# Kernel tuning notes

Measured on AMD Instinct MI355X. Metric: run time of the kernel, lower is better.

## Reference

```python
import jax, jax.numpy as jnp
import numpy as np

B, S, D, H = 4, 2048, 512, 8
DK = D // H


def setup_inputs() -> dict:
    key = jax.random.key(0)
    k1, k2, k3, k4 = jax.random.split(key, 4)
    return {
        "Zq": jax.random.normal(k1, (B, S, D), dtype=jnp.float32),
        "Zkv": jax.random.normal(k2, (B, S, D), dtype=jnp.float32),
        "mask": jnp.zeros((1, 1, S, S), dtype=jnp.float32),
        "Wqkv": jax.random.normal(k3, (D, 3 * D), dtype=jnp.float32),
        "Wout": jax.random.normal(k4, (D, D), dtype=jnp.float32),
    }


def reference(Zq, Zkv, mask, Wqkv, Wout):
    d_k = Wqkv.shape[0] // H
    Wq, Wk, Wv = jnp.split(Wqkv, 3, axis=-1)
    b, s, d = Zq.shape
    # project and split heads: [B,S,D] -> [B,H,S,dk]
    Q = (Zq @ Wq).reshape(b, s, H, d_k).transpose(0, 2, 1, 3)
    K = (Zkv @ Wk).reshape(b, s, H, d_k).transpose(0, 2, 1, 3)
    V = (Zkv @ Wv).reshape(b, s, H, d_k).transpose(0, 2, 1, 3)
    scale = d_k ** -0.5
    scores = jnp.einsum("bhqd,bhkd->bhqk", Q, K) * scale + mask
    attn = jax.nn.softmax(scores, axis=-1)  # [B,H,Sq,Skv]
    ctx = jnp.einsum("bhqk,bhkd->bhqd", attn, V)
    out = ctx.transpose(0, 2, 1, 3).reshape(b, s, d) @ Wout
    return out, attn.mean(axis=1)
```

## Files before the change

### kernel.cpp

```cpp
#include <hip/hip_runtime.h>
#include <cstdint>
#include <math.h>

#define B_ 4
#define S_ 2048
#define D_ 512
#define H_ 8
#define DK_ 64
#define SCALE 0.125f
#define INVLN2 1.4426950408889634f
#define QSCALE (SCALE * INVLN2)
#define KSTR 84
#define PSTR 68

using bfrag = __attribute__((ext_vector_type(8))) __bf16;
using b4    = __attribute__((ext_vector_type(4))) __bf16;
using f4    = __attribute__((ext_vector_type(4))) float;
using f2    = __attribute__((ext_vector_type(2))) float;
using f16v  = __attribute__((ext_vector_type(16))) float;
using u2    = __attribute__((ext_vector_type(2))) unsigned int;

#define MFMA16(a, b, c) __builtin_amdgcn_mfma_f32_16x16x32_bf16(a, b, c, 0, 0, 0)
#define MFMA32(a, b, c) __builtin_amdgcn_mfma_f32_32x32x16_bf16(a, b, c, 0, 0, 0)

__global__ __launch_bounds__(256) void wtr_all(
    const float* __restrict__ Wqkv, const float* __restrict__ Wout,
    __bf16* __restrict__ WqTh, __bf16* __restrict__ WqTl,
    __bf16* __restrict__ WkTh, __bf16* __restrict__ WkTl,
    __bf16* __restrict__ WvTh, __bf16* __restrict__ WoTh) {
  const int by = blockIdx.y;
  const int idx = blockIdx.x * 256 + threadIdx.x;
  const int k = idx & 511, n = idx >> 9;
  const float* W = (by == 3) ? Wout : Wqkv;
  const int ldw = (by == 3) ? 512 : 1536;
  const int c0 = (by == 3) ? 0 : by * 512;
  const float x = W[(size_t)k * ldw + c0 + n];
  const __bf16 h = (__bf16)x;
  __bf16* th = (by == 0) ? WqTh : (by == 1) ? WkTh : (by == 2) ? WvTh : WoTh;
  th[(size_t)n * 512 + k] = h;
  if (by < 2) {
    __bf16* tl = (by == 0) ? WqTl : WkTl;
    tl[(size_t)n * 512 + k] = (__bf16)(x - (float)h);
  }
}

__global__ __launch_bounds__(256) void qk_proj(
    const float* __restrict__ Zq, const float* __restrict__ Zkv,
    const __bf16* __restrict__ WqTh, const __bf16* __restrict__ WqTl,
    const __bf16* __restrict__ WkTh, const __bf16* __restrict__ WkTl,
    __bf16* __restrict__ Qh, __bf16* __restrict__ Ql,
    __bf16* __restrict__ Kh, __bf16* __restrict__ Kl) {
  __shared__ __bf16 Ash[64 * 40];
  __shared__ __bf16 Asl[64 * 40];
  __shared__ __bf16 Bsh[64 * 40];
  __shared__ __bf16 Bsl[64 * 40];

  const int zz = blockIdx.z;
  const float* A = zz ? Zkv : Zq;
  const __bf16* Bhp = zz ? WkTh : WqTh;
  const __bf16* Blp = zz ? WkTl : WqTl;
  __bf16* Oh = zz ? Kh : Qh;
  __bf16* Ol = zz ? Kl : Ql;
  const float cs = zz ? 1.0f : QSCALE;

  const int tid = threadIdx.x;
  const int m0 = blockIdx.y * 64, n0 = blockIdx.x * 64;
  const int row = tid >> 2, seg = tid & 3;
  const int lane = tid & 63, wv = tid >> 6;
  const int wm = (wv & 1) * 32, wn = (wv >> 1) * 32;
  const int qd = lane >> 4, ln = lane & 15;

  f4 acc[2][2];
#pragma unroll
  for (int i = 0; i < 2; i++)
#pragma unroll
    for (int j = 0; j < 2; j++)
#pragma unroll
      for (int r = 0; r < 4; r++) acc[i][j][r] = 0.f;

  for (int kt = 0; kt < 512; kt += 32) {
    const size_t abase = (size_t)(m0 + row) * 512 + kt + seg * 8;
    const size_t bbase = (size_t)(n0 + row) * 512 + kt + seg * 8;
    float4 a0 = *(const float4*)&A[abase];
    float4 a1 = *(const float4*)&A[abase + 4];
    float4 b0 = *(const float4*)&Bhp[bbase];
    float4 bl0 = *(const float4*)&Blp[bbase];
    __syncthreads();
    {
      float x[8] = {a0.x, a0.y, a0.z, a0.w, a1.x, a1.y, a1.z, a1.w};
      bfrag h, l;
#pragma unroll
      for (int j = 0; j < 8; j++) {
        h[j] = (__bf16)x[j];
        l[j] = (__bf16)(x[j] - (float)h[j]);
      }
      *(bfrag*)&Ash[row * 40 + seg * 8] = h;
      *(bfrag*)&Asl[row * 40 + seg * 8] = l;
    }
    *(float4*)&Bsh[row * 40 + seg * 8] = b0;
    *(float4*)&Bsl[row * 40 + seg * 8] = bl0;
    __syncthreads();

    bfrag ah[2], al[2], bh[2], bl[2];
#pragma unroll
    for (int mi = 0; mi < 2; mi++) {
      ah[mi] = *(bfrag*)&Ash[(wm + mi * 16 + ln) * 40 + qd * 8];
      al[mi] = *(bfrag*)&Asl[(wm + mi * 16 + ln) * 40 + qd * 8];
    }
#pragma unroll
    for (int ni = 0; ni < 2; ni++) {
      bh[ni] = *(bfrag*)&Bsh[(wn + ni * 16 + ln) * 40 + qd * 8];
      bl[ni] = *(bfrag*)&Bsl[(wn + ni * 16 + ln) * 40 + qd * 8];
    }
#pragma unroll
    for (int mi = 0; mi < 2; mi++)
#pragma unroll
      for (int ni = 0; ni < 2; ni++) {
        acc[mi][ni] = MFMA16(ah[mi], bh[ni], acc[mi][ni]);
        acc[mi][ni] = MFMA16(ah[mi], bl[ni], acc[mi][ni]);
        acc[mi][ni] = MFMA16(al[mi], bh[ni], acc[mi][ni]);
      }
  }

#pragma unroll
  for (int mi = 0; mi < 2; mi++)
#pragma unroll
    for (int ni = 0; ni < 2; ni++)
#pragma unroll
      for (int r = 0; r < 4; r++) {
        const int mrow = m0 + wm + mi * 16 + qd * 4 + r;
        const int ncol = n0 + wn + ni * 16 + ln;
        const float c = acc[mi][ni][r] * cs;
        const int b = mrow >> 11, s = mrow & (S_ - 1);
        const int h = ncol >> 6, dk = ncol & 63;
        const size_t o = (((size_t)b * H_ + h) * S_ + s) * DK_ + dk;
        __bf16 hh = (__bf16)c;
        Oh[o] = hh;
        Ol[o] = (__bf16)(c - (float)hh);
      }
}

template <bool AF32, bool BF32, bool LO, int MODE>
__global__ __launch_bounds__(256) void gemm_mfma(
    const void* __restrict__ Ap, const void* __restrict__ Bp, const void* __restrict__ Blop,
    float* __restrict__ Cf, __bf16* __restrict__ Oh, __bf16* __restrict__ Ol) {
  __shared__ __bf16 Ash[64 * 40];
  __shared__ __bf16 Asl[64 * 40];
  __shared__ __bf16 Bsh[64 * 40];
  __shared__ __bf16 Bsl[64 * 40];

  const int tid = threadIdx.x;
  const int m0 = blockIdx.y * 64, n0 = blockIdx.x * 64;
  const int row = tid >> 2, seg = tid & 3;
  const int lane = tid & 63, wv = tid >> 6;
  const int wm = (wv & 1) * 32, wn = (wv >> 1) * 32;
  const int qd = lane >> 4, ln = lane & 15;

  f4 acc[2][2];
#pragma unroll
  for (int i = 0; i < 2; i++)
#pragma unroll
    for (int j = 0; j < 2; j++)
#pragma unroll
      for (int r = 0; r < 4; r++) acc[i][j][r] = 0.f;

  for (int kt = 0; kt < 512; kt += 32) {
    const size_t abase = (size_t)(m0 + row) * 512 + kt + seg * 8;
    const size_t bbase = (size_t)(n0 + row) * 512 + kt + seg * 8;
    float4 a0, a1, b0, b1, bl0;
    if constexpr (AF32) {
      const float* A = (const float*)Ap;
      a0 = *(const float4*)&A[abase];
      a1 = *(const float4*)&A[abase + 4];
    } else {
      const __bf16* A = (const __bf16*)Ap;
      a0 = *(const float4*)&A[abase];
    }
    if constexpr (BF32) {
      const float* Bm = (const float*)Bp;
      b0 = *(const float4*)&Bm[bbase];
      b1 = *(const float4*)&Bm[bbase + 4];
    } else {
      const __bf16* Bm = (const __bf16*)Bp;
      b0 = *(const float4*)&Bm[bbase];
      if constexpr (LO) {
        const __bf16* Bl = (const __bf16*)Blop;
        bl0 = *(const float4*)&Bl[bbase];
      }
    }
    __syncthreads();
    if constexpr (AF32) {
      float x[8] = {a0.x, a0.y, a0.z, a0.w, a1.x, a1.y, a1.z, a1.w};
      bfrag h, l;
#pragma unroll
      for (int j = 0; j < 8; j++) {
        h[j] = (__bf16)x[j];
        l[j] = (__bf16)(x[j] - (float)h[j]);
      }
      *(bfrag*)&Ash[row * 40 + seg * 8] = h;
      if constexpr (LO) *(bfrag*)&Asl[row * 40 + seg * 8] = l;
    } else {
      *(float4*)&Ash[row * 40 + seg * 8] = a0;
    }
    if constexpr (BF32) {
      float x[8] = {b0.x, b0.y, b0.z, b0.w, b1.x, b1.y, b1.z, b1.w};
      bfrag h;
#pragma unroll
      for (int j = 0; j < 8; j++) h[j] = (__bf16)x[j];
      *(bfrag*)&Bsh[row * 40 + seg * 8] = h;
    } else {
      *(float4*)&Bsh[row * 40 + seg * 8] = b0;
      if constexpr (LO) *(float4*)&Bsl[row * 40 + seg * 8] = bl0;
    }
    __syncthreads();

    bfrag ah[2], al[2], bh[2], bl[2];
#pragma unroll
    for (int mi = 0; mi < 2; mi++) {
      ah[mi] = *(bfrag*)&Ash[(wm + mi * 16 + ln) * 40 + qd * 8];
      if constexpr (LO) al[mi] = *(bfrag*)&Asl[(wm + mi * 16 + ln) * 40 + qd * 8];
    }
#pragma unroll
    for (int ni = 0; ni < 2; ni++) {
      bh[ni] = *(bfrag*)&Bsh[(wn + ni * 16 + ln) * 40 + qd * 8];
      if constexpr (LO) bl[ni] = *(bfrag*)&Bsl[(wn + ni * 16 + ln) * 40 + qd * 8];
    }
#pragma unroll
    for (int mi = 0; mi < 2; mi++)
#pragma unroll
      for (int ni = 0; ni < 2; ni++) {
        acc[mi][ni] = MFMA16(ah[mi], bh[ni], acc[mi][ni]);
        if constexpr (LO) {
          acc[mi][ni] = MFMA16(ah[mi], bl[ni], acc[mi][ni]);
          acc[mi][ni] = MFMA16(al[mi], bh[ni], acc[mi][ni]);
        }
      }
  }

#pragma unroll
  for (int mi = 0; mi < 2; mi++)
#pragma unroll
    for (int ni = 0; ni < 2; ni++)
#pragma unroll
      for (int r = 0; r < 4; r++) {
        const int mrow = m0 + wm + mi * 16 + qd * 4 + r;
        const int ncol = n0 + wn + ni * 16 + ln;
        const float c = acc[mi][ni][r];
        if constexpr (MODE == 0) {
          Cf[(size_t)mrow * 512 + ncol] = c;
        } else if constexpr (MODE == 1) {
          const int b = mrow >> 11, s = mrow & (S_ - 1);
          const int h = ncol >> 6, dk = ncol & 63;
          const size_t o = (((size_t)b * H_ + h) * S_ + s) * DK_ + dk;
          __bf16 hh = (__bf16)c;
          Oh[o] = hh;
          Ol[o] = (__bf16)(c - (float)hh);
        } else {
          const int h = mrow >> 6, dk = mrow & 63;
          const int b = ncol >> 11, s = ncol & (S_ - 1);
          Oh[(((size_t)b * H_ + h) * DK_ + dk) * S_ + s] = (__bf16)c;
        }
      }
}

__global__ __launch_bounds__(256, 4) void attn_fctx(
    const __bf16* __restrict__ Qh_, const __bf16* __restrict__ Ql_,
    const __bf16* __restrict__ Kh_, const __bf16* __restrict__ Kl_,
    const __bf16* __restrict__ VT, const float* __restrict__ mask,
    __bf16* __restrict__ CTXb, float* __restrict__ MR, float* __restrict__ LR,
    unsigned char* __restrict__ E, float* __restrict__ MT) {
  __shared__ __bf16 Ksh[64 * KSTR];
  __shared__ __bf16 Ksl[64 * KSTR];
  __shared__ __bf16 Vs[64 * KSTR];
  __shared__ __bf16 Ps[128 * PSTR];
  __shared__ float als[128];
  const int tid = threadIdx.x, lane = tid & 63, wv = tid >> 6;
  const int l31 = lane & 31, kh = lane >> 5;
  const int qd = lane >> 4, ln = lane & 15;
  const int bh = blockIdx.y;
  const int q0b = blockIdx.x * 128;
  const int q0w = q0b + wv * 32;
  const int srow = tid >> 2, sseg = tid & 3;

  bfrag qhf[4], qlf[4];
#pragma unroll
  for (int ks = 0; ks < 4; ks++) {
    const size_t qb = ((size_t)bh * S_ + q0w + l31) * DK_ + ks * 16 + kh * 8;
    qhf[ks] = *(const bfrag*)&Qh_[qb];
    qlf[ks] = *(const bfrag*)&Ql_[qb];
  }

  float m = -3.0e38f, l = 0.f;
  f4 cacc[2][4];
#pragma unroll
  for (int mt = 0; mt < 2; mt++)
#pragma unroll
    for (int nt = 0; nt < 4; nt++)
#pragma unroll
      for (int r = 0; r < 4; r++) cacc[mt][nt][r] = 0.f;

  float4 h0, h1, l0, l1, v0, v1;
  {
    const size_t kb = ((size_t)bh * S_ + srow) * DK_ + sseg * 16;
    const size_t vb = ((size_t)bh * DK_ + srow) * S_ + sseg * 16;
    h0 = *(const float4*)&Kh_[kb]; h1 = *(const float4*)&Kh_[kb + 8];
    l0 = *(const float4*)&Kl_[kb]; l1 = *(const float4*)&Kl_[kb + 8];
    v0 = *(const float4*)&VT[vb];  v1 = *(const float4*)&VT[vb + 8];
  }

  for (int kt = 0; kt < S_; kt += 64) {
    __syncthreads();
    *(float4*)&Ksh[srow * KSTR + sseg * 16] = h0;
    *(float4*)&Ksh[srow * KSTR + sseg * 16 + 8] = h1;
    *(float4*)&Ksl[srow * KSTR + sseg * 16] = l0;
    *(float4*)&Ksl[srow * KSTR + sseg * 16 + 8] = l1;
    *(float4*)&Vs[srow * KSTR + sseg * 16] = v0;
    *(float4*)&Vs[srow * KSTR + sseg * 16 + 8] = v1;
    __syncthreads();

    f4 mk[2][4];
#pragma unroll
    for (int t = 0; t < 2; t++)
#pragma unroll
      for (int g = 0; g < 4; g++)
        mk[t][g] = *(const f4*)&mask[(size_t)(q0w + l31) * S_ + kt + t * 32 + g * 8 + 4 * kh];

    if (kt + 64 < S_) {
      const size_t kb = ((size_t)bh * S_ + kt + 64 + srow) * DK_ + sseg * 16;
      const size_t vb = ((size_t)bh * DK_ + srow) * S_ + kt + 64 + sseg * 16;
      h0 = *(const float4*)&Kh_[kb]; h1 = *(const float4*)&Kh_[kb + 8];
      l0 = *(const float4*)&Kl_[kb]; l1 = *(const float4*)&Kl_[kb + 8];
      v0 = *(const float4*)&VT[vb];  v1 = *(const float4*)&VT[vb + 8];
    }

    f16v z[2];
#pragma unroll
    for (int t = 0; t < 2; t++)
#pragma unroll
      for (int r = 0; r < 16; r++) z[t][r] = 0.f;
#pragma unroll
    for (int t = 0; t < 2; t++)
#pragma unroll
      for (int ks = 0; ks < 4; ks++) {
        bfrag kbh = *(bfrag*)&Ksh[(t * 32 + l31) * KSTR + ks * 16 + kh * 8];
        bfrag kbl = *(bfrag*)&Ksl[(t * 32 + l31) * KSTR + ks * 16 + kh * 8];
        z[t] = MFMA32(kbh, qhf[ks], z[t]);
        z[t] = MFMA32(kbl, qhf[ks], z[t]);
        z[t] = MFMA32(kbh, qlf[ks], z[t]);
      }

#pragma unroll
    for (int t = 0; t < 2; t++)
#pragma unroll
      for (int r = 0; r < 16; r++)
        z[t][r] = fmaf(mk[t][r >> 2][r & 3], INVLN2, z[t][r]);

    float tm = z[0][0];
#pragma unroll
    for (int t = 0; t < 2; t++)
#pragma unroll
      for (int r = 0; r < 16; r++) tm = fmaxf(tm, z[t][r]);
    tm = fmaxf(tm, __shfl_xor(tm, 32, 64));
    const bool need = (__any(tm > m) != 0);
    float al = 1.0f;
    if (need) {
      const float nm2 = fmaxf(m, tm);
      al = exp2f(m - nm2);
      m = nm2;
      if (lane < 32) als[wv * 32 + lane] = al;
    }
    const float nm = m;

    float ls = 0.f;
#pragma unroll
    for (int t = 0; t < 2; t++)
#pragma unroll
      for (int g = 0; g < 4; g++) {
        const float e0 = exp2f(z[t][g * 4 + 0] - nm);
        const float e1 = exp2f(z[t][g * 4 + 1] - nm);
        const float e2 = exp2f(z[t][g * 4 + 2] - nm);
        const float e3 = exp2f(z[t][g * 4 + 3] - nm);
        ls += (e0 + e1) + (e2 + e3);
        b4 pk;
        pk[0] = (__bf16)e0; pk[1] = (__bf16)e1;
        pk[2] = (__bf16)e2; pk[3] = (__bf16)e3;
        *(b4*)&Ps[(wv * 32 + l31) * PSTR + t * 32 + g * 8 + 4 * kh] = pk;
      }
    l = l * al + ls;

    if (lane < 32)
      MT[((size_t)bh * 32 + (kt >> 6)) * S_ + q0w + lane] = m;

    if (need) {
#pragma unroll
      for (int mt = 0; mt < 2; mt++) {
        f4 av = *(f4*)&als[wv * 32 + mt * 16 + qd * 4];
#pragma unroll
        for (int nt = 0; nt < 4; nt++)
#pragma unroll
          for (int r = 0; r < 4; r++) cacc[mt][nt][r] *= av[r];
      }
    }

    bfrag pa[2][2];
#pragma unroll
    for (int mt = 0; mt < 2; mt++)
#pragma unroll
      for (int ks = 0; ks < 2; ks++)
        pa[mt][ks] = *(bfrag*)&Ps[(wv * 32 + mt * 16 + ln) * PSTR + ks * 32 + qd * 8];
#pragma unroll
    for (int nt = 0; nt < 4; nt++)
#pragma unroll
      for (int ks = 0; ks < 2; ks++) {
        bfrag vbf = *(bfrag*)&Vs[(nt * 16 + ln) * KSTR + ks * 32 + qd * 8];
#pragma unroll
        for (int mt = 0; mt < 2; mt++)
          cacc[mt][nt] = MFMA16(pa[mt][ks], vbf, cacc[mt][nt]);
      }

#pragma unroll
    for (int c = 0; c < 4; c++) {
      const int row = wv * 32 + (lane >> 3) + c * 8;
      const int ch = lane & 7;
      bfrag pv = *(bfrag*)&Ps[row * PSTR + ch * 8];
      int lo = 0, hi = 0;
      lo = __builtin_amdgcn_cvt_pk_fp8_f32((float)pv[0], (float)pv[1], lo, 0);
      lo = __builtin_amdgcn_cvt_pk_fp8_f32((float)pv[2], (float)pv[3], lo, 1);
      hi = __builtin_amdgcn_cvt_pk_fp8_f32((float)pv[4], (float)pv[5], hi, 0);
      hi = __builtin_amdgcn_cvt_pk_fp8_f32((float)pv[6], (float)pv[7], hi, 1);
      u2 ev;
      ev.x = (unsigned int)lo;
      ev.y = (unsigned int)hi;
      __builtin_nontemporal_store(
          ev, (u2*)&E[((size_t)bh * S_ + q0b + row) * S_ + kt + ch * 8]);
    }
  }

  l += __shfl_xor(l, 32, 64);
  if (lane < 32) {
    MR[(size_t)bh * S_ + q0w + lane] = m;
    LR[(size_t)bh * S_ + q0w + lane] = l;
    als[wv * 32 + lane] = 1.0f / l;
  }
  const int b = bh >> 3, h = bh & 7;
#pragma unroll
  for (int mt = 0; mt < 2; mt++) {
    f4 iv = *(f4*)&als[wv * 32 + mt * 16 + qd * 4];
#pragma unroll
    for (int nt = 0; nt < 4; nt++)
#pragma unroll
      for (int r = 0; r < 4; r++)
        CTXb[((size_t)b * S_ + q0w + mt * 16 + qd * 4 + r) * D_ + h * DK_ + nt * 16 + ln] =
            (__bf16)(cacc[mt][nt][r] * iv[r]);
  }
}

__global__ __launch_bounds__(256) void mean_rescale(
    const unsigned char* __restrict__ E, const float* __restrict__ MT,
    const float* __restrict__ MR, const float* __restrict__ LR,
    float* __restrict__ meanout) {
  const int t = threadIdx.x;
  const int qr = t >> 3, seg = t & 7;
  const int b = blockIdx.y, ks = blockIdx.z;
  const int qg = blockIdx.x * 32 + qr;

  float mf[H_], il[H_];
#pragma unroll
  for (int h = 0; h < H_; h++) {
    const int bh = b * H_ + h;
    mf[h] = MR[(size_t)bh * S_ + qg];
    il[h] = 1.0f / LR[(size_t)bh * S_ + qg];
  }

  for (int kc = 0; kc < 8; kc++) {
    const int k0 = ks * 512 + kc * 64;
    const int tk = k0 >> 6;
    float acc[8];
#pragma unroll
    for (int j = 0; j < 8; j++) acc[j] = 0.f;
#pragma unroll
    for (int h = 0; h < H_; h++) {
      const int bh = b * H_ + h;
      const float mt = MT[((size_t)bh * 32 + tk) * S_ + qg];
      const float sc = exp2f(mt - mf[h]) * il[h];
      u2 e = __builtin_nontemporal_load(
          (const u2*)&E[((size_t)bh * S_ + qg) * S_ + k0 + seg * 8]);
      f2 p01 = __builtin_amdgcn_cvt_pk_f32_fp8((int)e.x, 0);
      f2 p23 = __builtin_amdgcn_cvt_pk_f32_fp8((int)e.x, 1);
      f2 p45 = __builtin_amdgcn_cvt_pk_f32_fp8((int)e.y, 0);
      f2 p67 = __builtin_amdgcn_cvt_pk_f32_fp8((int)e.y, 1);
      acc[0] += p01.x * sc; acc[1] += p01.y * sc;
      acc[2] += p23.x * sc; acc[3] += p23.y * sc;
      acc[4] += p45.x * sc; acc[5] += p45.y * sc;
      acc[6] += p67.x * sc; acc[7] += p67.y * sc;
    }
    f4 o0, o1;
    o0[0] = acc[0] * 0.125f; o0[1] = acc[1] * 0.125f;
    o0[2] = acc[2] * 0.125f; o0[3] = acc[3] * 0.125f;
    o1[0] = acc[4] * 0.125f; o1[1] = acc[5] * 0.125f;
    o1[2] = acc[6] * 0.125f; o1[3] = acc[7] * 0.125f;
    float* mp = &meanout[((size_t)b * S_ + qg) * S_ + k0 + seg * 8];
    *(f4*)&mp[0] = o0;
    *(f4*)&mp[4] = o1;
  }
}

extern "C" void kernel_launch(void* const* d_in, const int* in_sizes, int n_in,
                              void* d_out, int out_size, void* d_ws, size_t ws_size,
                              hipStream_t stream) {
  (void)in_sizes; (void)n_in; (void)out_size; (void)ws_size;
  const float* Zq = (const float*)d_in[0];
  const float* Zkv = (const float*)d_in[1];
  const float* mask = (const float*)d_in[2];
  const float* Wqkv = (const float*)d_in[3];
  const float* Wout = (const float*)d_in[4];

  float* out = (float*)d_out;
  float* mean = out + (size_t)B_ * S_ * D_;

  char* w = (char*)d_ws;
  const size_t WSZ = 512 * 512 * sizeof(__bf16);
  const size_t QSZ = (size_t)B_ * H_ * S_ * DK_ * sizeof(__bf16);
  __bf16* WqTh = (__bf16*)w; w += WSZ;
  __bf16* WqTl = (__bf16*)w; w += WSZ;
  __bf16* WkTh = (__bf16*)w; w += WSZ;
  __bf16* WkTl = (__bf16*)w; w += WSZ;
  __bf16* WvTh = (__bf16*)w; w += WSZ;
  __bf16* WoTh = (__bf16*)w; w += WSZ;
  __bf16* Qh = (__bf16*)w; w += QSZ;
  __bf16* Ql = (__bf16*)w; w += QSZ;
  __bf16* Kh = (__bf16*)w; w += QSZ;
  __bf16* Kl = (__bf16*)w; w += QSZ;
  __bf16* VTh = (__bf16*)w; w += QSZ;
  __bf16* CTXb = (__bf16*)w; w += QSZ;
  float* MR = (float*)w; w += (size_t)B_ * H_ * S_ * sizeof(float);
  float* LR = (float*)w; w += (size_t)B_ * H_ * S_ * sizeof(float);
  float* MT = (float*)w; w += (size_t)B_ * H_ * 32 * S_ * sizeof(float);
  unsigned char* E = (unsigned char*)w; w += (size_t)B_ * H_ * S_ * S_;

  wtr_all<<<dim3(1024, 4), 256, 0, stream>>>(Wqkv, Wout, WqTh, WqTl, WkTh, WkTl, WvTh, WoTh);

  qk_proj<<<dim3(8, 128, 2), 256, 0, stream>>>(
      Zq, Zkv, WqTh, WqTl, WkTh, WkTl, Qh, Ql, Kh, Kl);
  gemm_mfma<false, true, false, 2><<<dim3(128, 8), 256, 0, stream>>>(
      WvTh, Zkv, nullptr, nullptr, VTh, nullptr);

  attn_fctx<<<dim3(16, 32), 256, 0, stream>>>(Qh, Ql, Kh, Kl, VTh, mask, CTXb, MR, LR, E, MT);
  mean_rescale<<<dim3(64, 4, 4), 256, 0, stream>>>(E, MT, MR, LR, mean);

  gemm_mfma<false, false, false, 0><<<dim3(8, 128), 256, 0, stream>>>(
      CTXb, WoTh, nullptr, out, nullptr, nullptr);
}
```

Measured before the change: 456.1 us.

## Process attention K tile in two 32-column halves to cut live registers

Splits the 64-key inner step of the flash attention kernel into two 32-key sub-steps, each doing its own mask load, score MFMA, online-softmax update and PV accumulation. This lowers how many score and mask registers are live at once, and the launch-bounds hint drops from 4 to 3 waves per SIMD. The per-tile running max is now recorded at 32-key granularity, so MT doubles in size and mean_rescale indexes it per half-tile. The conditional skip of the rescale is removed, so the accumulator is rescaled every sub-step, which adds ALU work and doubles the MT writes and the shuffle/max reductions.

New measurement: 497.0 us. 1.09x slower.

```diff
diff --git a/kernel.cpp b/kernel.cpp
--- a/kernel.cpp
+++ b/kernel.cpp
@@ -263,7 +263,7 @@
       }
 }
 
-__global__ __launch_bounds__(256, 4) void attn_fctx(
+__global__ __launch_bounds__(256, 3) void attn_fctx(
     const __bf16* __restrict__ Qh_, const __bf16* __restrict__ Ql_,
     const __bf16* __restrict__ Kh_, const __bf16* __restrict__ Kl_,
     const __bf16* __restrict__ VT, const float* __restrict__ mask,
@@ -318,13 +318,6 @@
     *(float4*)&Vs[srow * KSTR + sseg * 16 + 8] = v1;
     __syncthreads();
 
-    f4 mk[2][4];
-#pragma unroll
-    for (int t = 0; t < 2; t++)
-#pragma unroll
-      for (int g = 0; g < 4; g++)
-        mk[t][g] = *(const f4*)&mask[(size_t)(q0w + l31) * S_ + kt + t * 32 + g * 8 + 4 * kh];
-
     if (kt + 64 < S_) {
       const size_t kb = ((size_t)bh * S_ + kt + 64 + srow) * DK_ + sseg * 16;
       const size_t vb = ((size_t)bh * DK_ + srow) * S_ + kt + 64 + sseg * 16;
@@ -333,65 +326,56 @@
       v0 = *(const float4*)&VT[vb];  v1 = *(const float4*)&VT[vb + 8];
     }
 
-    f16v z[2];
-#pragma unroll
-    for (int t = 0; t < 2; t++)
-#pragma unroll
-      for (int r = 0; r < 16; r++) z[t][r] = 0.f;
-#pragma unroll
-    for (int t = 0; t < 2; t++)
+#pragma unroll
+    for (int t = 0; t < 2; t++) {
+      f4 mk[4];
+#pragma unroll
+      for (int g = 0; g < 4; g++)
+        mk[g] = *(const f4*)&mask[(size_t)(q0w + l31) * S_ + kt + t * 32 + g * 8 + 4 * kh];
+
+      f16v z;
+#pragma unroll
+      for (int r = 0; r < 16; r++) z[r] = 0.f;
 #pragma unroll
       for (int ks = 0; ks < 4; ks++) {
         bfrag kbh = *(bfrag*)&Ksh[(t * 32 + l31) * KSTR + ks * 16 + kh * 8];
         bfrag kbl = *(bfrag*)&Ksl[(t * 32 + l31) * KSTR + ks * 16 + kh * 8];
-        z[t] = MFMA32(kbh, qhf[ks], z[t]);
-        z[t] = MFMA32(kbl, qhf[ks], z[t]);
-        z[t] = MFMA32(kbh, qlf[ks], z[t]);
-      }
-
-#pragma unroll
-    for (int t = 0; t < 2; t++)
+        z = MFMA32(kbh, qhf[ks], z);
+        z = MFMA32(kbl, qhf[ks], z);
+        z = MFMA32(kbh, qlf[ks], z);
+      }
+
 #pragma unroll
       for (int r = 0; r < 16; r++)
-        z[t][r] = fmaf(mk[t][r >> 2][r & 3], INVLN2, z[t][r]);
-
-    float tm = z[0][0];
-#pragma unroll
-    for (int t = 0; t < 2; t++)
-#pragma unroll
-      for (int r = 0; r < 16; r++) tm = fmaxf(tm, z[t][r]);
-    tm = fmaxf(tm, __shfl_xor(tm, 32, 64));
-    const bool need = (__any(tm > m) != 0);
-    float al = 1.0f;
-    if (need) {
-      const float nm2 = fmaxf(m, tm);
-      al = exp2f(m - nm2);
-      m = nm2;
+        z[r] = fmaf(mk[r >> 2][r & 3], INVLN2, z[r]);
+
+      float tm = z[0];
+#pragma unroll
+      for (int r = 1; r < 16; r++) tm = fmaxf(tm, z[r]);
+      tm = fmaxf(tm, __shfl_xor(tm, 32, 64));
+      const float nm = fmaxf(m, tm);
+      const float al = exp2f(m - nm);
+      m = nm;
       if (lane < 32) als[wv * 32 + lane] = al;
-    }
-    const float nm = m;
-
-    float ls = 0.f;
-#pragma unroll
-    for (int t = 0; t < 2; t++)
+
+      float ls = 0.f;
 #pragma unroll
       for (int g = 0; g < 4; g++) {
-        const float e0 = exp2f(z[t][g * 4 + 0] - nm);
-        const float e1 = exp2f(z[t][g * 4 + 1] - nm);
-        const float e2 = exp2f(z[t][g * 4 + 2] - nm);
-        const float e3 = exp2f(z[t][g * 4 + 3] - nm);
+        const float e0 = exp2f(z[g * 4 + 0] - nm);
+        const float e1 = exp2f(z[g * 4 + 1] - nm);
+        const float e2 = exp2f(z[g * 4 + 2] - nm);
+        const float e3 = exp2f(z[g * 4 + 3] - nm);
         ls += (e0 + e1) + (e2 + e3);
         b4 pk;
         pk[0] = (__bf16)e0; pk[1] = (__bf16)e1;
         pk[2] = (__bf16)e2; pk[3] = (__bf16)e3;
         *(b4*)&Ps[(wv * 32 + l31) * PSTR + t * 32 + g * 8 + 4 * kh] = pk;
       }
-    l = l * al + ls;
-
-    if (lane < 32)
-      MT[((size_t)bh * 32 + (kt >> 6)) * S_ + q0w + lane] = m;
-
-    if (need) {
+      l = l * al + ls;
+
+      if (lane < 32)
+        MT[((size_t)bh * 64 + (kt >> 5) + t) * S_ + q0w + lane] = m;
+
 #pragma unroll
       for (int mt = 0; mt < 2; mt++) {
         f4 av = *(f4*)&als[wv * 32 + mt * 16 + qd * 4];
@@ -400,23 +384,19 @@
 #pragma unroll
           for (int r = 0; r < 4; r++) cacc[mt][nt][r] *= av[r];
       }
-    }
-
-    bfrag pa[2][2];
-#pragma unroll
-    for (int mt = 0; mt < 2; mt++)
-#pragma unroll
-      for (int ks = 0; ks < 2; ks++)
-        pa[mt][ks] = *(bfrag*)&Ps[(wv * 32 + mt * 16 + ln) * PSTR + ks * 32 + qd * 8];
-#pragma unroll
-    for (int nt = 0; nt < 4; nt++)
-#pragma unroll
-      for (int ks = 0; ks < 2; ks++) {
-        bfrag vbf = *(bfrag*)&Vs[(nt * 16 + ln) * KSTR + ks * 32 + qd * 8];
+
+      bfrag pa[2];
+#pragma unroll
+      for (int mt = 0; mt < 2; mt++)
+        pa[mt] = *(bfrag*)&Ps[(wv * 32 + mt * 16 + ln) * PSTR + t * 32 + qd * 8];
+#pragma unroll
+      for (int nt = 0; nt < 4; nt++) {
+        bfrag vbf = *(bfrag*)&Vs[(nt * 16 + ln) * KSTR + t * 32 + qd * 8];
 #pragma unroll
         for (int mt = 0; mt < 2; mt++)
-          cacc[mt][nt] = MFMA16(pa[mt][ks], vbf, cacc[mt][nt]);
-      }
+          cacc[mt][nt] = MFMA16(pa[mt], vbf, cacc[mt][nt]);
+      }
+    }
 
 #pragma unroll
     for (int c = 0; c < 4; c++) {
@@ -474,14 +454,14 @@
 
   for (int kc = 0; kc < 8; kc++) {
     const int k0 = ks * 512 + kc * 64;
-    const int tk = k0 >> 6;
+    const int tk2 = (k0 >> 5) + (seg >> 2);
     float acc[8];
 #pragma unroll
     for (int j = 0; j < 8; j++) acc[j] = 0.f;
 #pragma unroll
     for (int h = 0; h < H_; h++) {
       const int bh = b * H_ + h;
-      const float mt = MT[((size_t)bh * 32 + tk) * S_ + qg];
+      const float mt = MT[((size_t)bh * 64 + tk2) * S_ + qg];
       const float sc = exp2f(mt - mf[h]) * il[h];
       u2 e = __builtin_nontemporal_load(
           (const u2*)&E[((size_t)bh * S_ + qg) * S_ + k0 + seg * 8]);
@@ -535,7 +515,7 @@
   __bf16* CTXb = (__bf16*)w; w += QSZ;
   float* MR = (float*)w; w += (size_t)B_ * H_ * S_ * sizeof(float);
   float* LR = (float*)w; w += (size_t)B_ * H_ * S_ * sizeof(float);
-  float* MT = (float*)w; w += (size_t)B_ * H_ * 32 * S_ * sizeof(float);
+  float* MT = (float*)w; w += (size_t)B_ * H_ * 64 * S_ * sizeof(float);
   unsigned char* E = (unsigned char*)w; w += (size_t)B_ * H_ * S_ * S_;
 
   wtr_all<<<dim3(1024, 4), 256, 0, stream>>>(Wqkv, Wout, WqTh, WqTl, WkTh, WkTl, WvTh, WoTh);
```
